# Performance work log

Measured on AMD Instinct MI355X. Metric: run time of the kernel, lower is better.

## Reference

```python
import jax, jax.numpy as jnp
import numpy as np

WINDOW = 512  # window_size from init_kwargs


def _sliding_window_attn(q, k, v, window):
    # q,k,v: [B, S, H, D]; each query attends to keys j with i-window < j <= i (causal band)
    B, S, H, D = q.shape
    W = window
    NB = S // W  # S chosen divisible by W
    qb = q.reshape(B, NB, W, H, D)
    kb = k.reshape(B, NB, W, H, D)
    vb = v.reshape(B, NB, W, H, D)
    # previous block of keys/values (zeros for block 0, masked out below)
    kprev = jnp.pad(kb, ((0, 0), (1, 0), (0, 0), (0, 0), (0, 0)))[:, :NB]
    vprev = jnp.pad(vb, ((0, 0), (1, 0), (0, 0), (0, 0), (0, 0)))[:, :NB]
    kcat = jnp.concatenate([kprev, kb], axis=2)  # [B, NB, 2W, H, D]
    vcat = jnp.concatenate([vprev, vb], axis=2)
    qi = jnp.arange(W)
    kj = jnp.arange(2 * W) - W  # key position relative to block start
    rel = kj[None, :] - qi[:, None]  # [W, 2W]
    win_mask = (rel <= 0) & (rel > -W)  # causal window of size W (incl. self)
    blk = jnp.arange(NB)
    valid_key = (blk[:, None, None] > 0) | (kj[None, None, :] >= 0)  # block 0 has no prev
    mask = win_mask[None] & valid_key  # [NB, W, 2W]
    scale = 1.0 / np.sqrt(D).astype(np.float32)
    scores = jnp.einsum('bnqhd,bnkhd->bhnqk', qb, kcat) * scale  # [B,H,NB,W,2W]
    scores = jnp.where(mask[None, None], scores, jnp.finfo(scores.dtype).min)
    probs = jax.nn.softmax(scores, axis=-1)
    out = jnp.einsum('bhnqk,bnkhd->bnqhd', probs, vcat)  # [B,NB,W,H,D]
    return out.reshape(B, S, H, D)


def setup_inputs() -> dict:
    B, S, H, D = 2, 8192, 8, 64
    root = jax.random.key(0)
    k1, k2, k3, k4, k5 = jax.random.split(root, 5)
    query = jax.random.normal(k1, (B, S, H, D), dtype=jnp.float32)
    key = jax.random.normal(k2, (B, S, H, D), dtype=jnp.float32)
    value = jax.random.normal(k3, (B, S, H, D), dtype=jnp.float32)
    W_out = jax.random.normal(k4, (H * D, H * D), dtype=jnp.float32) * (1.0 / np.sqrt(H * D))
    b_out = jax.random.normal(k5, (H * D,), dtype=jnp.float32) * 0.01
    return {'query': query, 'key': key, 'value': value, 'W_out': W_out, 'b_out': b_out}


def reference(query, key, value, W_out, b_out):
    B, S, H, D = query.shape
    # seq_len (8192) > window_size (512) -> sliding-window branch of the module
    attn = _sliding_window_attn(query, key, value, WINDOW)
    flat = attn.reshape(B, S, H * D)
    # out_proj (nn.Linear); dropout=0.0 is identity; no attention_mask
    return flat @ W_out.T + b_out
```

## Files before the change

### kernel.cpp

```cpp
#include <hip/hip_runtime.h>

#define B_ 2
#define S_ 8192
#define H_ 8
#define D_ 64
#define HD_ 512
#define WIN_ 512

typedef __bf16 bf16x8 __attribute__((ext_vector_type(8)));
typedef float f32x4 __attribute__((ext_vector_type(4)));
typedef unsigned short u16;
typedef unsigned int u32;

__device__ __forceinline__ u16 f2bf(float f) {
  u32 u = __float_as_uint(f);
  u += 0x7FFFu + ((u >> 16) & 1u);
  return (u16)(u >> 16);
}

__device__ __forceinline__ bf16x8 cvt8s(const float* p, float s) {
  const float4 a = *(const float4*)p;
  const float4 b = *(const float4*)(p + 4);
  union { u16 s[8]; bf16x8 v; } r;
  r.s[0] = f2bf(a.x * s); r.s[1] = f2bf(a.y * s); r.s[2] = f2bf(a.z * s); r.s[3] = f2bf(a.w * s);
  r.s[4] = f2bf(b.x * s); r.s[5] = f2bf(b.y * s); r.s[6] = f2bf(b.z * s); r.s[7] = f2bf(b.w * s);
  return r.v;
}

#define MFMA(a, b, c) __builtin_amdgcn_mfma_f32_16x16x32_bf16(a, b, c, 0, 0, 0)

__global__ __launch_bounds__(256) void vtrans_kernel(const float* __restrict__ v,
                                                     u16* __restrict__ vt) {
  const int t = threadIdx.x;
  const int s0 = (blockIdx.x & (S_ / 64 - 1)) * 64;
  const int bh = blockIdx.x >> 7;
  const int b = bh >> 3, h = bh & 7;
  __shared__ float tile[64][65];
#pragma unroll
  for (int it = 0; it < 16; ++it) {
    int idx = it * 256 + t;
    int r = idx >> 6, c = idx & 63;
    tile[r][c] = v[((size_t)(b * S_ + s0 + r) * H_ + h) * D_ + c];
  }
  __syncthreads();
#pragma unroll
  for (int it = 0; it < 16; ++it) {
    int idx = it * 256 + t;
    int dd = idx >> 6, c = idx & 63;
    vt[((size_t)(b * H_ + h) * D_ + dd) * S_ + s0 + c] = f2bf(tile[c][dd]);
  }
}

__global__ __launch_bounds__(256) void cvt_kernel(const float* __restrict__ in,
                                                  u16* __restrict__ out, int n4) {
  int i = blockIdx.x * 256 + threadIdx.x;
  if (i < n4) {
    float4 f = ((const float4*)in)[i];
    ushort4 r;
    r.x = f2bf(f.x); r.y = f2bf(f.y); r.z = f2bf(f.z); r.w = f2bf(f.w);
    ((ushort4*)out)[i] = r;
  }
}

__global__ __launch_bounds__(512) void attn_kernel(const float* __restrict__ q,
                                                   const u16* __restrict__ kb,
                                                   const u16* __restrict__ vt,
                                                   u16* __restrict__ attn) {
  const int tid = threadIdx.x;
  const int lane = tid & 63;
  const int wave = tid >> 6;
  const int lg = lane >> 4;
  const int lj = lane & 15;
  const int bid = (int)blockIdx.x;
  const int swz = (bid & 7) * 128 + (bid >> 3);
  const int qc = swz & 63;
  const int bh = swz >> 6;
  const int b = bh >> 3, h = bh & 7;
  const int q0blk = qc * 128;
  const int q0w = q0blk + wave * 16;

  __shared__ __align__(16) u16 klds0[32 * 64], klds1[32 * 64];
  __shared__ __align__(16) u16 vlds0[64 * 32], vlds1[64 * 32];
  __shared__ __align__(16) u16 plds[8][16 * 36];

  const float qscale = 0.125f * 1.4426950408889634f;
  bf16x8 aq0, aq1;
  {
    const float* qrow = q + ((size_t)(b * S_ + q0w + lj) * H_ + h) * D_;
    aq0 = cvt8s(qrow + lg * 8, qscale);
    aq1 = cvt8s(qrow + 32 + lg * 8, qscale);
  }

  f32x4 o0 = {0.f, 0.f, 0.f, 0.f}, o1 = o0, o2 = o0, o3 = o0;
  float lacc[4] = {0.f, 0.f, 0.f, 0.f};

  const int tbw = (q0w >= WIN_) ? ((q0w - (WIN_ - 1)) >> 5) : 0;
  const int tew = (q0w + 15) >> 5;
  const int tbu = (q0blk >= WIN_) ? ((q0blk - (WIN_ - 1)) >> 5) : 0;
  const int teu = (q0blk + 127) >> 5;
  const bool wmask = (q0w >= WIN_);

  const bool isK = (wave < 4);
  const u16* gbase;
  size_t gstep;
  u16 *l0, *l1;
  if (isK) {
    const int chunk = wave * 64 + lane;
    const int r = chunk >> 3, c = chunk & 7;
    gbase = kb + ((size_t)(b * S_ + r) * H_ + h) * D_ + c * 8;
    gstep = (size_t)32 * HD_;
    const int dst = r * 64 + ((c * 8) ^ ((r & 7) << 3));
    l0 = klds0 + dst; l1 = klds1 + dst;
  } else {
    const int chunk = (wave - 4) * 64 + lane;
    const int d = chunk >> 2, c = chunk & 3;
    gbase = vt + ((size_t)(b * H_ + h) * D_ + d) * S_ + c * 8;
    gstep = 32;
    const int dst = d * 32 + ((c * 8) ^ ((d & 3) << 3));
    l0 = vlds0 + dst; l1 = vlds1 + dst;
  }

  const int ko0 = lj * 64 + ((lg * 8) ^ ((lj & 7) << 3));
  const int ko1 = lj * 64 + (((32 + lg * 8)) ^ ((lj & 7) << 3));
  const int vo = lj * 32 + ((lg * 8) ^ ((lj & 3) << 3));
  const int po = lj * 36 + lg * 8;

  {
    uint4 g0 = *(const uint4*)(gbase + gstep * tbu);
    *(uint4*)l0 = g0;
  }
  uint4 greg;
  if (tbu < teu) greg = *(const uint4*)(gbase + gstep * (tbu + 1));
  __syncthreads();

  int cur = 0;
  for (int t = tbu; t <= teu; ++t) {
    if (t >= tbw && t <= tew) {
      const u16* K = cur ? klds1 : klds0;
      const u16* V = cur ? vlds1 : vlds0;
      bf16x8 k00 = *(const bf16x8*)(K + ko0);
      bf16x8 k01 = *(const bf16x8*)(K + ko1);
      bf16x8 k10 = *(const bf16x8*)(K + ko0 + 1024);
      bf16x8 k11 = *(const bf16x8*)(K + ko1 + 1024);

      f32x4 sA = {0.f, 0.f, 0.f, 0.f}, sB = sA;
      sA = MFMA(aq0, k00, sA);
      sA = MFMA(aq1, k01, sA);
      sB = MFMA(aq0, k10, sB);
      sB = MFMA(aq1, k11, sB);

      const bool edge = (t == tew) || (wmask && t == tbw);
      u16* ps = &plds[wave][0];
#pragma unroll
      for (int r = 0; r < 4; ++r) {
        float ea = __builtin_amdgcn_exp2f(sA[r]);
        float eb = __builtin_amdgcn_exp2f(sB[r]);
        if (edge) {
          const int qpos = q0w + lg * 4 + r;
          const int kA = 32 * t + lj, kB = kA + 16;
          const bool okA = (kA <= qpos) && (kA > qpos - WIN_);
          const bool okB = (kB <= qpos) && (kB > qpos - WIN_);
          ea = okA ? ea : 0.f;
          eb = okB ? eb : 0.f;
        }
        lacc[r] += ea + eb;
        ps[(lg * 4 + r) * 36 + lj] = (u16)(__float_as_uint(ea) >> 16);
        ps[(lg * 4 + r) * 36 + 16 + lj] = (u16)(__float_as_uint(eb) >> 16);
      }
      bf16x8 ap = *(const bf16x8*)(ps + po);

      bf16x8 v0 = *(const bf16x8*)(V + vo);
      bf16x8 v1 = *(const bf16x8*)(V + vo + 512);
      bf16x8 v2 = *(const bf16x8*)(V + vo + 1024);
      bf16x8 v3 = *(const bf16x8*)(V + vo + 1536);
      o0 = MFMA(ap, v0, o0);
      o1 = MFMA(ap, v1, o1);
      o2 = MFMA(ap, v2, o2);
      o3 = MFMA(ap, v3, o3);
    }

    if (t < teu) {
      u16* dst = cur ? l0 : l1;
      *(uint4*)dst = greg;
    }
    __syncthreads();
    if (t + 1 < teu) greg = *(const uint4*)(gbase + gstep * (t + 2));
    cur ^= 1;
  }

#pragma unroll
  for (int r = 0; r < 4; ++r) {
    float l = lacc[r];
    l += __shfl_xor(l, 1);
    l += __shfl_xor(l, 2);
    l += __shfl_xor(l, 4);
    l += __shfl_xor(l, 8);
    const float inv = 1.0f / l;
    const int row = q0w + lg * 4 + r;
    u16* orow = attn + (size_t)(b * S_ + row) * HD_ + h * D_;
    orow[lj] = f2bf(o0[r] * inv);
    orow[16 + lj] = f2bf(o1[r] * inv);
    orow[32 + lj] = f2bf(o2[r] * inv);
    orow[48 + lj] = f2bf(o3[r] * inv);
  }
}

__global__ __launch_bounds__(512) void gemm_kernel(const u16* __restrict__ A,
                                                   const u16* __restrict__ Wb,
                                                   const float* __restrict__ bias,
                                                   float* __restrict__ out) {
  const int tid = threadIdx.x;
  const int lane = tid & 63;
  const int wave = tid >> 6;
  const int lg = lane >> 4, lj = lane & 15;
  const int phys = (int)blockIdx.x;
  const int swz = (phys & 7) * 32 + (phys >> 3);
  const int rb = swz >> 1, cb = swz & 1;
  const int wr = wave >> 2, wc = wave & 3;
  const int row0 = rb * 128;
  const int col0 = cb * 256 + wc * 64;

  __shared__ __align__(16) u16 alds[2][128 * 64];

  const int srow = tid >> 3;
  const int skc = tid & 7;
  const u16* ag0 = A + (size_t)(row0 + srow) * HD_ + skc * 8;
  const u16* ag1 = A + (size_t)(row0 + 64 + srow) * HD_ + skc * 8;
  const int dst0 = srow * 64 + ((skc * 8) ^ ((srow & 7) << 3));
  const int dst1 = (64 + srow) * 64 + ((skc * 8) ^ ((srow & 7) << 3));

  f32x4 acc[4][4];
#pragma unroll
  for (int fr = 0; fr < 4; ++fr)
#pragma unroll
    for (int fc = 0; fc < 4; ++fc) acc[fr][fc] = (f32x4){0.f, 0.f, 0.f, 0.f};

  *(uint4*)(&alds[0][dst0]) = *(const uint4*)ag0;
  *(uint4*)(&alds[0][dst1]) = *(const uint4*)ag1;
  __syncthreads();

  uint4 pre0, pre1;
  int cur = 0;
  for (int kt = 0; kt < HD_; kt += 64) {
    if (kt + 64 < HD_) {
      pre0 = *(const uint4*)(ag0 + kt + 64);
      pre1 = *(const uint4*)(ag1 + kt + 64);
    }
    const u16* Abuf = alds[cur];
#pragma unroll
    for (int ks = 0; ks < 2; ++ks) {
      bf16x8 fa[4], fb[4];
#pragma unroll
      for (int fr = 0; fr < 4; ++fr) {
        const int rr = wr * 64 + fr * 16 + lj;
        fa[fr] = *(const bf16x8*)(Abuf + rr * 64 + ((ks * 32 + lg * 8) ^ ((lj & 7) << 3)));
      }
#pragma unroll
      for (int fc = 0; fc < 4; ++fc)
        fb[fc] = *(const bf16x8*)(Wb + (size_t)(col0 + fc * 16 + lj) * HD_ + kt + ks * 32 + lg * 8);
#pragma unroll
      for (int fr = 0; fr < 4; ++fr)
#pragma unroll
        for (int fc = 0; fc < 4; ++fc)
          acc[fr][fc] = MFMA(fa[fr], fb[fc], acc[fr][fc]);
    }
    if (kt + 64 < HD_) {
      u16* db = alds[cur ^ 1];
      *(uint4*)(&db[dst0]) = pre0;
      *(uint4*)(&db[dst1]) = pre1;
    }
    __syncthreads();
    cur ^= 1;
  }

#pragma unroll
  for (int fc = 0; fc < 4; ++fc) {
    const float bv = bias[col0 + fc * 16 + lj];
#pragma unroll
    for (int fr = 0; fr < 4; ++fr) {
#pragma unroll
      for (int r = 0; r < 4; ++r) {
        const int row = row0 + wr * 64 + fr * 16 + lg * 4 + r;
        out[(size_t)row * HD_ + col0 + fc * 16 + lj] = acc[fr][fc][r] + bv;
      }
    }
  }
}

extern "C" void kernel_launch(void* const* d_in, const int* in_sizes, int n_in,
                              void* d_out, int out_size, void* d_ws, size_t ws_size,
                              hipStream_t stream) {
  const float* q = (const float*)d_in[0];
  const float* k = (const float*)d_in[1];
  const float* v = (const float*)d_in[2];
  const float* w = (const float*)d_in[3];
  const float* bias = (const float*)d_in[4];
  float* out = (float*)d_out;

  char* ws = (char*)d_ws;
  u16* vt = (u16*)ws;
  u16* kbb = (u16*)(ws + 16777216);
  u16* attn = (u16*)(ws + 33554432);
  u16* wb = (u16*)(ws + 50331648);

  hipLaunchKernelGGL(vtrans_kernel, dim3(2048), dim3(256), 0, stream, v, vt);
  hipLaunchKernelGGL(cvt_kernel, dim3(8192), dim3(256), 0, stream, k, kbb, 2097152);
  hipLaunchKernelGGL(cvt_kernel, dim3(256), dim3(256), 0, stream, w, wb, 65536);
  hipLaunchKernelGGL(attn_kernel, dim3(1024), dim3(512), 0, stream, q, kbb, vt, attn);
  hipLaunchKernelGGL(gemm_kernel, dim3(256), dim3(512), 0, stream, attn, wb, bias, out);
}
```

Measured before the change: 103.6 us.

## Fuse K/V bf16 conversion and V transpose into attention tile loads

Removes the separate V-transpose and K-conversion kernels. The attention kernel now reads fp32 K and V directly, converts them to bf16 in registers, and writes K as packed vectors and V as a transposed scatter into LDS. This saves two launches and the round trip through the workspace, but doubles the global bytes per tile load and turns the V LDS writes into scalar 16-bit stores. It also pads the P staging row stride from 36 to 40 elements.

```diff
diff --git a/kernel.cpp b/kernel.cpp
--- a/kernel.cpp
+++ b/kernel.cpp
@@ -28,28 +28,6 @@
 }
 
 #define MFMA(a, b, c) __builtin_amdgcn_mfma_f32_16x16x32_bf16(a, b, c, 0, 0, 0)
-
-__global__ __launch_bounds__(256) void vtrans_kernel(const float* __restrict__ v,
-                                                     u16* __restrict__ vt) {
-  const int t = threadIdx.x;
-  const int s0 = (blockIdx.x & (S_ / 64 - 1)) * 64;
-  const int bh = blockIdx.x >> 7;
-  const int b = bh >> 3, h = bh & 7;
-  __shared__ float tile[64][65];
-#pragma unroll
-  for (int it = 0; it < 16; ++it) {
-    int idx = it * 256 + t;
-    int r = idx >> 6, c = idx & 63;
-    tile[r][c] = v[((size_t)(b * S_ + s0 + r) * H_ + h) * D_ + c];
-  }
-  __syncthreads();
-#pragma unroll
-  for (int it = 0; it < 16; ++it) {
-    int idx = it * 256 + t;
-    int dd = idx >> 6, c = idx & 63;
-    vt[((size_t)(b * H_ + h) * D_ + dd) * S_ + s0 + c] = f2bf(tile[c][dd]);
-  }
-}
 
 __global__ __launch_bounds__(256) void cvt_kernel(const float* __restrict__ in,
                                                   u16* __restrict__ out, int n4) {
@@ -63,8 +41,8 @@
 }
 
 __global__ __launch_bounds__(512) void attn_kernel(const float* __restrict__ q,
-                                                   const u16* __restrict__ kb,
-                                                   const u16* __restrict__ vt,
+                                                   const float* __restrict__ kf,
+                                                   const float* __restrict__ vf,
                                                    u16* __restrict__ attn) {
   const int tid = threadIdx.x;
   const int lane = tid & 63;
@@ -81,7 +59,7 @@
 
   __shared__ __align__(16) u16 klds0[32 * 64], klds1[32 * 64];
   __shared__ __align__(16) u16 vlds0[64 * 32], vlds1[64 * 32];
-  __shared__ __align__(16) u16 plds[8][16 * 36];
+  __shared__ __align__(16) u16 plds[8][16 * 40];
 
   const float qscale = 0.125f * 1.4426950408889634f;
   bf16x8 aq0, aq1;
@@ -101,36 +79,55 @@
   const bool wmask = (q0w >= WIN_);
 
   const bool isK = (wave < 4);
-  const u16* gbase;
-  size_t gstep;
+  const float* gf;
+  const size_t gstepf = (size_t)32 * H_ * D_;
   u16 *l0, *l1;
+  int vkey = 0, vd0 = 0;
   if (isK) {
     const int chunk = wave * 64 + lane;
     const int r = chunk >> 3, c = chunk & 7;
-    gbase = kb + ((size_t)(b * S_ + r) * H_ + h) * D_ + c * 8;
-    gstep = (size_t)32 * HD_;
+    gf = kf + ((size_t)(b * S_ + r) * H_ + h) * D_ + c * 8;
     const int dst = r * 64 + ((c * 8) ^ ((r & 7) << 3));
     l0 = klds0 + dst; l1 = klds1 + dst;
   } else {
-    const int chunk = (wave - 4) * 64 + lane;
-    const int d = chunk >> 2, c = chunk & 3;
-    gbase = vt + ((size_t)(b * H_ + h) * D_ + d) * S_ + c * 8;
-    gstep = 32;
-    const int dst = d * 32 + ((c * 8) ^ ((d & 3) << 3));
-    l0 = vlds0 + dst; l1 = vlds1 + dst;
-  }
+    const int u = (wave - 4) * 64 + lane;
+    vkey = u & 31;
+    vd0 = (u >> 5) * 8;
+    gf = vf + ((size_t)(b * S_ + vkey) * H_ + h) * D_ + vd0;
+    l0 = vlds0; l1 = vlds1;
+  }
+
+  auto kpack = [](float4 a, float4 c) {
+    union { u16 s[8]; uint4 q; } t;
+    t.s[0] = f2bf(a.x); t.s[1] = f2bf(a.y); t.s[2] = f2bf(a.z); t.s[3] = f2bf(a.w);
+    t.s[4] = f2bf(c.x); t.s[5] = f2bf(c.y); t.s[6] = f2bf(c.z); t.s[7] = f2bf(c.w);
+    return t.q;
+  };
+  auto vscatter = [&](u16* vb, float4 a, float4 c) {
+    float vals[8] = {a.x, a.y, a.z, a.w, c.x, c.y, c.z, c.w};
+#pragma unroll
+    for (int i = 0; i < 8; ++i) {
+      const int d = vd0 + i;
+      vb[d * 32 + (vkey ^ ((d & 3) << 3))] = f2bf(vals[i]);
+    }
+  };
 
   const int ko0 = lj * 64 + ((lg * 8) ^ ((lj & 7) << 3));
   const int ko1 = lj * 64 + (((32 + lg * 8)) ^ ((lj & 7) << 3));
   const int vo = lj * 32 + ((lg * 8) ^ ((lj & 3) << 3));
-  const int po = lj * 36 + lg * 8;
+  const int po = lj * 40 + lg * 8;
 
   {
-    uint4 g0 = *(const uint4*)(gbase + gstep * tbu);
-    *(uint4*)l0 = g0;
-  }
-  uint4 greg;
-  if (tbu < teu) greg = *(const uint4*)(gbase + gstep * (tbu + 1));
+    float4 a = *(const float4*)(gf + gstepf * tbu);
+    float4 c = *(const float4*)(gf + gstepf * tbu + 4);
+    if (isK) *(uint4*)l0 = kpack(a, c);
+    else vscatter(vlds0, a, c);
+  }
+  float4 ga, gb;
+  if (tbu < teu) {
+    ga = *(const float4*)(gf + gstepf * (tbu + 1));
+    gb = *(const float4*)(gf + gstepf * (tbu + 1) + 4);
+  }
   __syncthreads();
 
   int cur = 0;
@@ -164,8 +161,8 @@
           eb = okB ? eb : 0.f;
         }
         lacc[r] += ea + eb;
-        ps[(lg * 4 + r) * 36 + lj] = (u16)(__float_as_uint(ea) >> 16);
-        ps[(lg * 4 + r) * 36 + 16 + lj] = (u16)(__float_as_uint(eb) >> 16);
+        ps[(lg * 4 + r) * 40 + lj] = (u16)(__float_as_uint(ea) >> 16);
+        ps[(lg * 4 + r) * 40 + 16 + lj] = (u16)(__float_as_uint(eb) >> 16);
       }
       bf16x8 ap = *(const bf16x8*)(ps + po);
 
@@ -180,11 +177,18 @@
     }
 
     if (t < teu) {
-      u16* dst = cur ? l0 : l1;
-      *(uint4*)dst = greg;
+      if (isK) {
+        u16* dst = cur ? l0 : l1;
+        *(uint4*)dst = kpack(ga, gb);
+      } else {
+        vscatter(cur ? vlds0 : vlds1, ga, gb);
+      }
     }
     __syncthreads();
-    if (t + 1 < teu) greg = *(const uint4*)(gbase + gstep * (t + 2));
+    if (t + 1 < teu) {
+      ga = *(const float4*)(gf + gstepf * (t + 2));
+      gb = *(const float4*)(gf + gstepf * (t + 2) + 4);
+    }
     cur ^= 1;
   }
 
@@ -298,14 +302,10 @@
   float* out = (float*)d_out;
 
   char* ws = (char*)d_ws;
-  u16* vt = (u16*)ws;
-  u16* kbb = (u16*)(ws + 16777216);
-  u16* attn = (u16*)(ws + 33554432);
-  u16* wb = (u16*)(ws + 50331648);
-
-  hipLaunchKernelGGL(vtrans_kernel, dim3(2048), dim3(256), 0, stream, v, vt);
-  hipLaunchKernelGGL(cvt_kernel, dim3(8192), dim3(256), 0, stream, k, kbb, 2097152);
+  u16* attn = (u16*)ws;
+  u16* wb = (u16*)(ws + 16777216);
+
   hipLaunchKernelGGL(cvt_kernel, dim3(256), dim3(256), 0, stream, w, wb, 65536);
-  hipLaunchKernelGGL(attn_kernel, dim3(1024), dim3(512), 0, stream, q, kbb, vt, attn);
+  hipLaunchKernelGGL(attn_kernel, dim3(1024), dim3(512), 0, stream, q, k, v, attn);
   hipLaunchKernelGGL(gemm_kernel, dim3(256), dim3(512), 0, stream, attn, wb, bias, out);
 }
```

Measured after the change: 85.53 us. -17.4%, faster.
